# Kernel optimization log

Measured on AMD Instinct MI355X. Metric: run time of the kernel, lower is better.

## Reference

```python
import jax, jax.numpy as jnp
import numpy as np

# Izhikevich constants (module defaults)
A, B_P, C_P, D_P = 0.02, 0.2, -65.0, 8.0
V_TH, DT, T_STEPS = 30.0, 0.5, 8
LN_EPS = 1e-5

IN_F, OUT_F, BATCH = 4096, 4096, 256


def setup_inputs() -> dict:
    key = jax.random.key(0)
    k_x, k_w, k_n = jax.random.split(key, 3)
    x = jax.random.normal(k_x, (BATCH, IN_F), dtype=jnp.float32)
    # kaiming_normal_ fan_in / relu: std = sqrt(2 / fan_in)
    W = jax.random.normal(k_w, (OUT_F, IN_F), dtype=jnp.float32) * np.sqrt(2.0 / IN_F)
    b = jnp.zeros((OUT_F,), dtype=jnp.float32)
    ln_gamma = jnp.ones((OUT_F,), dtype=jnp.float32)
    ln_beta = jnp.zeros((OUT_F,), dtype=jnp.float32)
    current_mag = jnp.asarray(12.0, dtype=jnp.float32)
    # per-step injected noise, precomputed for determinism: (T, B, N)
    noise = jax.random.normal(k_n, (T_STEPS, BATCH, OUT_F), dtype=jnp.float32)
    return {"x": x, "W": W, "b": b, "ln_gamma": ln_gamma, "ln_beta": ln_beta,
            "current_mag": current_mag, "noise": noise}


@jax.custom_vjp
def superspike(v):
    return (v >= V_TH).astype(v.dtype)

def _ss_fwd(v):
    return superspike(v), v

def _ss_bwd(v, g):
    return (g / (1.0 + jnp.abs(v - V_TH)) ** 2,)

superspike.defvjp(_ss_fwd, _ss_bwd)


def reference(x, W, b, ln_gamma, ln_beta, current_mag, noise):
    # 1. Linear projection: (B, in) @ (in, out)
    raw = x @ W.T + b
    # 2. LayerNorm -> tanh -> scale to pA range
    mu = jnp.mean(raw, axis=-1, keepdims=True)
    var = jnp.mean(jnp.square(raw - mu), axis=-1, keepdims=True)
    ln = (raw - mu) * jax.lax.rsqrt(var + LN_EPS) * ln_gamma + ln_beta
    I_inj = jnp.tanh(ln) * jnp.abs(current_mag)  # (B, N)

    B = x.shape[0]
    v0 = jnp.full((B, OUT_F), -65.0, dtype=x.dtype)
    u0 = jnp.full((B, OUT_F), B_P * -65.0, dtype=x.dtype)

    def step(carry, noise_t):
        v, u = carry
        I_t = I_inj + 0.3 * noise_t
        dv = (0.04 * v * v + 5.0 * v + 140.0 - u + I_t) * DT
        du = A * (B_P * v - u) * DT
        v_new = jnp.clip(v + dv, -100.0, 60.0)
        u_new = jnp.clip(u + du, -100.0, 100.0)
        s = superspike(v_new)
        v_out = v_new * (1.0 - s) + C_P * s
        u_out = u_new + D_P * s
        # truncated BPTT: detach state each step
        new_carry = (jax.lax.stop_gradient(v_out), jax.lax.stop_gradient(u_out))
        return new_carry, s

    _, spikes = jax.lax.scan(step, (v0, u0), noise)  # spikes: (T, B, N)
    return jnp.sum(spikes, axis=0) / T_STEPS
```

## Files before the change

kernel.cpp:

```cpp
#include <hip/hip_runtime.h>
#include <math.h>

#define IN_F 4096
#define OUT_F 4096
#define BATCH 256
#define TSTEPS 8

#define BM 128
#define BN 64
#define BK 32
#define KSPLIT 8
#define KLEN (IN_F / KSPLIT)
#define NKT (KLEN / BK)
#define LDA 40

typedef _Float16 f16x8 __attribute__((ext_vector_type(8)));
typedef float f32x4 __attribute__((ext_vector_type(4)));

__device__ __forceinline__ void cvt8(const float4 a, const float4 b,
                                     f16x8& h0, f16x8& h1) {
  const float v[8] = {a.x, a.y, a.z, a.w, b.x, b.y, b.z, b.w};
#pragma unroll
  for (int j = 0; j < 8; ++j) {
    const float sv = v[j] * 64.0f;
    const _Float16 c0 = (_Float16)sv;
    const float r = (sv - (float)c0) * 2048.0f;
    h0[j] = c0;
    h1[j] = (_Float16)r;
  }
}

__global__ __launch_bounds__(256, 3) void gemm_split(
    const float* __restrict__ X, const float* __restrict__ Wt,
    float* __restrict__ out) {
  __shared__ __align__(16) _Float16 B0s[BN][LDA];
  __shared__ __align__(16) _Float16 B1s[BN][LDA];

  const int tid = threadIdx.x;
  const int lane = tid & 63;
  const int w = tid >> 6;
  const int lr = lane & 15;
  const int lk = lane >> 4;

  const int m0 = blockIdx.y * BM;
  const int n0 = blockIdx.x * BN;
  const int kbeg = blockIdx.z * KLEN;

  const float* paf0 = X + (size_t)(m0 + w * 32 + lr) * IN_F + kbeg + lk * 8;
  const float* paf1 = paf0 + (size_t)16 * IN_F;

  const int brow = tid >> 2;
  const int bko = (tid & 3) * 8;
  const float* pb = Wt + (size_t)(n0 + brow) * IN_F + kbeg + bko;

  f32x4 acc0[2][4], acc1[2][4];
#pragma unroll
  for (int i = 0; i < 2; ++i)
#pragma unroll
    for (int j = 0; j < 4; ++j) {
      acc0[i][j] = (f32x4){0.f, 0.f, 0.f, 0.f};
      acc1[i][j] = (f32x4){0.f, 0.f, 0.f, 0.f};
    }

  float4 b0 = *(const float4*)(pb);
  float4 b1 = *(const float4*)(pb + 4);

  for (int kt = 0; kt < NKT; ++kt) {
    const int ko = kt * BK;
    const float4 a00 = *(const float4*)(paf0 + ko);
    const float4 a01 = *(const float4*)(paf0 + ko + 4);
    const float4 a10 = *(const float4*)(paf1 + ko);
    const float4 a11 = *(const float4*)(paf1 + ko + 4);

    __syncthreads();
    {
      f16x8 h0, h1;
      cvt8(b0, b1, h0, h1);
      *(f16x8*)&B0s[brow][bko] = h0;
      *(f16x8*)&B1s[brow][bko] = h1;
    }
    if (kt + 1 < NKT) {
      b0 = *(const float4*)(pb + ko + BK);
      b1 = *(const float4*)(pb + ko + BK + 4);
    }
    __syncthreads();

    f16x8 fa0[2], fa1[2];
    cvt8(a00, a01, fa0[0], fa1[0]);
    cvt8(a10, a11, fa0[1], fa1[1]);

#pragma unroll
    for (int j = 0; j < 4; ++j) {
      const f16x8 fb0 = *(const f16x8*)&B0s[j * 16 + lr][lk * 8];
      const f16x8 fb1 = *(const f16x8*)&B1s[j * 16 + lr][lk * 8];
#pragma unroll
      for (int i = 0; i < 2; ++i) {
        acc0[i][j] = __builtin_amdgcn_mfma_f32_16x16x32_f16(fa0[i], fb0, acc0[i][j], 0, 0, 0);
        acc1[i][j] = __builtin_amdgcn_mfma_f32_16x16x32_f16(fa0[i], fb1, acc1[i][j], 0, 0, 0);
        acc1[i][j] = __builtin_amdgcn_mfma_f32_16x16x32_f16(fa1[i], fb0, acc1[i][j], 0, 0, 0);
      }
    }
  }

#pragma unroll
  for (int i = 0; i < 2; ++i) {
    const int rbase = m0 + w * 32 + i * 16 + lk * 4;
#pragma unroll
    for (int j = 0; j < 4; ++j) {
      const int c = n0 + j * 16 + lr;
#pragma unroll
      for (int r = 0; r < 4; ++r) {
        const float val = acc0[i][j][r] * 2.44140625e-4f  +
                          acc1[i][j][r] * 1.1920928955078125e-7f ;
        atomicAdd(&out[(size_t)(rbase + r) * OUT_F + c], val);
      }
    }
  }
}

__global__ __launch_bounds__(512) void snn_fused(
    float* __restrict__ raw, const float* __restrict__ bias,
    const float* __restrict__ gamma, const float* __restrict__ beta,
    const float* __restrict__ cmag, const float* __restrict__ noise) {
  const int row = blockIdx.x;
  const int tid = threadIdx.x;
  const int lane = tid & 63;
  const int wid = tid >> 6;
  const int col = tid * 8;
  __shared__ float redS[8], redQ[8];

  float x[8];
#pragma unroll
  for (int p = 0; p < 2; ++p) {
    const float4 rv = *(const float4*)&raw[(size_t)row * OUT_F + col + p * 4];
    const float4 bv = *(const float4*)&bias[col + p * 4];
    x[p * 4 + 0] = rv.x + bv.x;
    x[p * 4 + 1] = rv.y + bv.y;
    x[p * 4 + 2] = rv.z + bv.z;
    x[p * 4 + 3] = rv.w + bv.w;
  }
  float s = 0.f, q = 0.f;
#pragma unroll
  for (int e = 0; e < 8; ++e) {
    s += x[e];
    q += x[e] * x[e];
  }
#pragma unroll
  for (int off = 32; off; off >>= 1) {
    s += __shfl_xor(s, off);
    q += __shfl_xor(q, off);
  }
  if (lane == 0) {
    redS[wid] = s;
    redQ[wid] = q;
  }
  __syncthreads();
  s = 0.f;
  q = 0.f;
#pragma unroll
  for (int wv = 0; wv < 8; ++wv) {
    s += redS[wv];
    q += redQ[wv];
  }
  const float mu = s * (1.0f / (float)OUT_F);
  const float var = q * (1.0f / (float)OUT_F) - mu * mu;
  const float sc = 1.0f / sqrtf(var + 1e-5f);
  const float mag = fabsf(cmag[0]);

  float I[8];
#pragma unroll
  for (int p = 0; p < 2; ++p) {
    const float4 g = *(const float4*)&gamma[col + p * 4];
    const float4 be = *(const float4*)&beta[col + p * 4];
    I[p * 4 + 0] = tanhf((x[p * 4 + 0] - mu) * sc * g.x + be.x) * mag;
    I[p * 4 + 1] = tanhf((x[p * 4 + 1] - mu) * sc * g.y + be.y) * mag;
    I[p * 4 + 2] = tanhf((x[p * 4 + 2] - mu) * sc * g.z + be.z) * mag;
    I[p * 4 + 3] = tanhf((x[p * 4 + 3] - mu) * sc * g.w + be.w) * mag;
  }

  float v[8], u[8];
  int cnt[8];
#pragma unroll
  for (int j = 0; j < 8; ++j) {
    v[j] = -65.0f;
    u[j] = -13.0f;
    cnt[j] = 0;
  }

#pragma unroll
  for (int t = 0; t < TSTEPS; ++t) {
    float nn[8];
#pragma unroll
    for (int p = 0; p < 2; ++p) {
      const float4 nz = *(const float4*)&noise[(((size_t)t * BATCH) + row) * OUT_F + col + p * 4];
      nn[p * 4 + 0] = nz.x;
      nn[p * 4 + 1] = nz.y;
      nn[p * 4 + 2] = nz.z;
      nn[p * 4 + 3] = nz.w;
    }
#pragma unroll
    for (int j = 0; j < 8; ++j) {
      const float It = I[j] + 0.3f * nn[j];
      const float vv = v[j];
      const float dv = (0.04f * vv * vv + 5.0f * vv + 140.0f - u[j] + It) * 0.5f;
      const float du = 0.02f * (0.2f * vv - u[j]) * 0.5f;
      float vn = vv + dv;
      vn = fminf(fmaxf(vn, -100.0f), 60.0f);
      float un = u[j] + du;
      un = fminf(fmaxf(un, -100.0f), 100.0f);
      const bool sp = (vn >= 30.0f);
      v[j] = sp ? -65.0f : vn;
      u[j] = sp ? (un + 8.0f) : un;
      cnt[j] += sp ? 1 : 0;
    }
  }

#pragma unroll
  for (int p = 0; p < 2; ++p) {
    float4 o;
    o.x = (float)cnt[p * 4 + 0] * 0.125f;
    o.y = (float)cnt[p * 4 + 1] * 0.125f;
    o.z = (float)cnt[p * 4 + 2] * 0.125f;
    o.w = (float)cnt[p * 4 + 3] * 0.125f;
    *(float4*)&raw[(size_t)row * OUT_F + col + p * 4] = o;
  }
}

extern "C" void kernel_launch(void* const* d_in, const int* in_sizes, int n_in,
                              void* d_out, int out_size, void* d_ws, size_t ws_size,
                              hipStream_t stream) {
  const float* x = (const float*)d_in[0];
  const float* W = (const float*)d_in[1];
  const float* b = (const float*)d_in[2];
  const float* gam = (const float*)d_in[3];
  const float* bet = (const float*)d_in[4];
  const float* cmag = (const float*)d_in[5];
  const float* nz = (const float*)d_in[6];
  float* out = (float*)d_out;
  (void)d_ws;
  (void)ws_size;

  hipMemsetAsync(out, 0, (size_t)BATCH * OUT_F * sizeof(float), stream);

  dim3 grid1(OUT_F / BN, BATCH / BM, KSPLIT);
  gemm_split<<<grid1, 256, 0, stream>>>(x, W, out);

  snn_fused<<<BATCH, 512, 0, stream>>>(out, b, gam, bet, cmag, nz);
}
```

Measured before the change: 186.4 us.

## Pre-split X into fp16 planes and stream W directly without LDS

A new pre-pass kernel splits X once into high and low fp16 planes in the workspace. The GEMM now uses 512-thread blocks that cover the whole batch, so W is read once per block instead of once per M-tile. The LDS staging of B and its barriers are removed: each wave loads its W fragments from global memory and converts them in registers. In exchange, every wave repeats the W fp32-to-fp16 split, and the pre-pass adds one extra launch plus a write and read of the X planes.

```diff
diff --git a/kernel.cpp b/kernel.cpp
--- a/kernel.cpp
+++ b/kernel.cpp
@@ -6,13 +6,11 @@
 #define BATCH 256
 #define TSTEPS 8
 
-#define BM 128
 #define BN 64
 #define BK 32
 #define KSPLIT 8
 #define KLEN (IN_F / KSPLIT)
 #define NKT (KLEN / BK)
-#define LDA 40
 
 typedef _Float16 f16x8 __attribute__((ext_vector_type(8)));
 typedef float f32x4 __attribute__((ext_vector_type(4)));
@@ -30,28 +28,37 @@
   }
 }
 
-__global__ __launch_bounds__(256, 3) void gemm_split(
-    const float* __restrict__ X, const float* __restrict__ Wt,
-    float* __restrict__ out) {
-  __shared__ __align__(16) _Float16 B0s[BN][LDA];
-  __shared__ __align__(16) _Float16 B1s[BN][LDA];
-
+__global__ __launch_bounds__(256) void split_x(const float* __restrict__ X,
+                                               _Float16* __restrict__ h0p,
+                                               _Float16* __restrict__ h1p) {
+  const size_t idx = ((size_t)blockIdx.x * 256 + threadIdx.x) * 8;
+  const float4 a = *(const float4*)&X[idx];
+  const float4 b = *(const float4*)&X[idx + 4];
+  f16x8 h0, h1;
+  cvt8(a, b, h0, h1);
+  *(f16x8*)&h0p[idx] = h0;
+  *(f16x8*)&h1p[idx] = h1;
+}
+
+template <bool USE_WS>
+__global__ void gemm_stream(const _Float16* __restrict__ Ah0,
+                            const _Float16* __restrict__ Ah1,
+                            const float* __restrict__ X,
+                            const float* __restrict__ Wt,
+                            float* __restrict__ out) {
   const int tid = threadIdx.x;
   const int lane = tid & 63;
   const int w = tid >> 6;
   const int lr = lane & 15;
   const int lk = lane >> 4;
 
-  const int m0 = blockIdx.y * BM;
   const int n0 = blockIdx.x * BN;
   const int kbeg = blockIdx.z * KLEN;
 
-  const float* paf0 = X + (size_t)(m0 + w * 32 + lr) * IN_F + kbeg + lk * 8;
-  const float* paf1 = paf0 + (size_t)16 * IN_F;
-
-  const int brow = tid >> 2;
-  const int bko = (tid & 3) * 8;
-  const float* pb = Wt + (size_t)(n0 + brow) * IN_F + kbeg + bko;
+  const _Float16* pa0 = Ah0 + (size_t)(w * 32 + lr) * IN_F + kbeg + lk * 8;
+  const _Float16* pa1 = Ah1 + (size_t)(w * 32 + lr) * IN_F + kbeg + lk * 8;
+  const float* pax = X + (size_t)(w * 32 + lr) * IN_F + kbeg + lk * 8;
+  const float* pb = Wt + (size_t)(n0 + lr) * IN_F + kbeg + lk * 8;
 
   f32x4 acc0[2][4], acc1[2][4];
 #pragma unroll
@@ -62,37 +69,32 @@
       acc1[i][j] = (f32x4){0.f, 0.f, 0.f, 0.f};
     }
 
-  float4 b0 = *(const float4*)(pb);
-  float4 b1 = *(const float4*)(pb + 4);
-
+#pragma unroll 4
   for (int kt = 0; kt < NKT; ++kt) {
     const int ko = kt * BK;
-    const float4 a00 = *(const float4*)(paf0 + ko);
-    const float4 a01 = *(const float4*)(paf0 + ko + 4);
-    const float4 a10 = *(const float4*)(paf1 + ko);
-    const float4 a11 = *(const float4*)(paf1 + ko + 4);
-
-    __syncthreads();
-    {
-      f16x8 h0, h1;
-      cvt8(b0, b1, h0, h1);
-      *(f16x8*)&B0s[brow][bko] = h0;
-      *(f16x8*)&B1s[brow][bko] = h1;
-    }
-    if (kt + 1 < NKT) {
-      b0 = *(const float4*)(pb + ko + BK);
-      b1 = *(const float4*)(pb + ko + BK + 4);
-    }
-    __syncthreads();
 
     f16x8 fa0[2], fa1[2];
-    cvt8(a00, a01, fa0[0], fa1[0]);
-    cvt8(a10, a11, fa0[1], fa1[1]);
+    if (USE_WS) {
+      fa0[0] = *(const f16x8*)(pa0 + ko);
+      fa0[1] = *(const f16x8*)(pa0 + (size_t)16 * IN_F + ko);
+      fa1[0] = *(const f16x8*)(pa1 + ko);
+      fa1[1] = *(const f16x8*)(pa1 + (size_t)16 * IN_F + ko);
+    } else {
+      const float4 a00 = *(const float4*)(pax + ko);
+      const float4 a01 = *(const float4*)(pax + ko + 4);
+      const float4 a10 = *(const float4*)(pax + (size_t)16 * IN_F + ko);
+      const float4 a11 = *(const float4*)(pax + (size_t)16 * IN_F + ko + 4);
+      cvt8(a00, a01, fa0[0], fa1[0]);
+      cvt8(a10, a11, fa0[1], fa1[1]);
+    }
 
 #pragma unroll
     for (int j = 0; j < 4; ++j) {
-      const f16x8 fb0 = *(const f16x8*)&B0s[j * 16 + lr][lk * 8];
-      const f16x8 fb1 = *(const f16x8*)&B1s[j * 16 + lr][lk * 8];
+      const float* pbj = pb + (size_t)(j * 16) * IN_F + ko;
+      const float4 b0 = *(const float4*)(pbj);
+      const float4 b1 = *(const float4*)(pbj + 4);
+      f16x8 fb0, fb1;
+      cvt8(b0, b1, fb0, fb1);
 #pragma unroll
       for (int i = 0; i < 2; ++i) {
         acc0[i][j] = __builtin_amdgcn_mfma_f32_16x16x32_f16(fa0[i], fb0, acc0[i][j], 0, 0, 0);
@@ -104,7 +106,7 @@
 
 #pragma unroll
   for (int i = 0; i < 2; ++i) {
-    const int rbase = m0 + w * 32 + i * 16 + lk * 4;
+    const int rbase = w * 32 + i * 16 + lk * 4;
 #pragma unroll
     for (int j = 0; j < 4; ++j) {
       const int c = n0 + j * 16 + lr;
@@ -237,13 +239,21 @@
   const float* cmag = (const float*)d_in[5];
   const float* nz = (const float*)d_in[6];
   float* out = (float*)d_out;
-  (void)d_ws;
-  (void)ws_size;
 
   hipMemsetAsync(out, 0, (size_t)BATCH * OUT_F * sizeof(float), stream);
 
-  dim3 grid1(OUT_F / BN, BATCH / BM, KSPLIT);
-  gemm_split<<<grid1, 256, 0, stream>>>(x, W, out);
+  const size_t plane_elems = (size_t)BATCH * IN_F;
+  const bool use_ws = ws_size >= 2 * plane_elems * sizeof(_Float16);
+
+  dim3 grid1(OUT_F / BN, 1, KSPLIT);
+  if (use_ws) {
+    _Float16* ah0 = (_Float16*)d_ws;
+    _Float16* ah1 = ah0 + plane_elems;
+    split_x<<<plane_elems / (256 * 8), 256, 0, stream>>>(x, ah0, ah1);
+    gemm_stream<true><<<grid1, 512, 0, stream>>>(ah0, ah1, x, W, out);
+  } else {
+    gemm_stream<false><<<grid1, 512, 0, stream>>>(nullptr, nullptr, x, W, out);
+  }
 
   snn_fused<<<BATCH, 512, 0, stream>>>(out, b, gam, bet, cmag, nz);
 }
```

Result: slower. 241.8 us (+29.7%).

## Restructure split-K GEMM to full-batch tiles with X staged in swizzled LDS

Applied to the files above, without the earlier changes.

The GEMM now has each 512-thread block cover all 256 batch rows by 128 output columns of one K slice, for a grid of 256 blocks. X is converted to a split fp16 pair and staged in a 64KB XOR-swizzled LDS buffer. W fragments are loaded straight from global memory into registers and double-buffered across the MFMA sequence. This removes the W conversion that each M-tile used to repeat, and it reuses the X tile across 128 columns. The cost is a larger accumulator footprint (32 f32x4 per thread), 64KB of LDS per block and fewer blocks, which together may cut occupancy and latency hiding.

```diff
diff --git a/kernel.cpp b/kernel.cpp
--- a/kernel.cpp
+++ b/kernel.cpp
@@ -6,13 +6,8 @@
 #define BATCH 256
 #define TSTEPS 8
 
-#define BM 128
-#define BN 64
-#define BK 32
 #define KSPLIT 8
 #define KLEN (IN_F / KSPLIT)
-#define NKT (KLEN / BK)
-#define LDA 40
 
 typedef _Float16 f16x8 __attribute__((ext_vector_type(8)));
 typedef float f32x4 __attribute__((ext_vector_type(4)));
@@ -30,92 +25,118 @@
   }
 }
 
-__global__ __launch_bounds__(256, 3) void gemm_split(
+__global__ __launch_bounds__(512, 2) void gemm_fused(
     const float* __restrict__ X, const float* __restrict__ Wt,
     float* __restrict__ out) {
-  __shared__ __align__(16) _Float16 B0s[BN][LDA];
-  __shared__ __align__(16) _Float16 B1s[BN][LDA];
+  __shared__ __align__(16) char Al[65536];
 
   const int tid = threadIdx.x;
   const int lane = tid & 63;
   const int w = tid >> 6;
+  const int mq = w & 3;
+  const int ng = w >> 2;
   const int lr = lane & 15;
   const int lk = lane >> 4;
 
-  const int m0 = blockIdx.y * BM;
-  const int n0 = blockIdx.x * BN;
-  const int kbeg = blockIdx.z * KLEN;
-
-  const float* paf0 = X + (size_t)(m0 + w * 32 + lr) * IN_F + kbeg + lk * 8;
-  const float* paf1 = paf0 + (size_t)16 * IN_F;
-
-  const int brow = tid >> 2;
-  const int bko = (tid & 3) * 8;
-  const float* pb = Wt + (size_t)(n0 + brow) * IN_F + kbeg + bko;
-
-  f32x4 acc0[2][4], acc1[2][4];
-#pragma unroll
-  for (int i = 0; i < 2; ++i)
+  const int nb = blockIdx.x & 31;
+  const int ksl = blockIdx.x >> 5;
+  const int n0 = nb * 128;
+  const int kbeg = ksl * KLEN;
+
+  const int srow = tid >> 1;
+  const int skh = (tid & 1) * 32;
+  const float* px = X + (size_t)srow * IN_F + kbeg + skh;
+
+  const float* pw = Wt + (size_t)(n0 + ng * 64 + lr) * IN_F + kbeg + lk * 8;
+
+  f32x4 acc0[4][4], acc1[4][4];
+#pragma unroll
+  for (int i = 0; i < 4; ++i)
 #pragma unroll
     for (int j = 0; j < 4; ++j) {
       acc0[i][j] = (f32x4){0.f, 0.f, 0.f, 0.f};
       acc1[i][j] = (f32x4){0.f, 0.f, 0.f, 0.f};
     }
 
-  float4 b0 = *(const float4*)(pb);
-  float4 b1 = *(const float4*)(pb + 4);
-
-  for (int kt = 0; kt < NKT; ++kt) {
-    const int ko = kt * BK;
-    const float4 a00 = *(const float4*)(paf0 + ko);
-    const float4 a01 = *(const float4*)(paf0 + ko + 4);
-    const float4 a10 = *(const float4*)(paf1 + ko);
-    const float4 a11 = *(const float4*)(paf1 + ko + 4);
-
+  float4 Apre[8];
+#pragma unroll
+  for (int c = 0; c < 8; ++c) Apre[c] = *(const float4*)(px + c * 4);
+
+#define LOADW2(P, JT) \
+  do { \
+    P[0] = *(const float4*)(pwst + (size_t)(JT) * 16 * IN_F); \
+    P[1] = *(const float4*)(pwst + (size_t)(JT) * 16 * IN_F + 4); \
+  } while (0)
+
+#define COMPUTE2(P, JT) \
+  do { \
+    f16x8 fb0, fb1; \
+    cvt8(P[0], P[1], fb0, fb1); \
+    _Pragma("unroll") for (int i_ = 0; i_ < 4; ++i_) { \
+      acc0[i_][JT] = __builtin_amdgcn_mfma_f32_16x16x32_f16(fa0[i_], fb0, acc0[i_][JT], 0, 0, 0); \
+      acc1[i_][JT] = __builtin_amdgcn_mfma_f32_16x16x32_f16(fa0[i_], fb1, acc1[i_][JT], 0, 0, 0); \
+      acc1[i_][JT] = __builtin_amdgcn_mfma_f32_16x16x32_f16(fa1[i_], fb0, acc1[i_][JT], 0, 0, 0); \
+    } \
+  } while (0)
+
+  for (int st = 0; st < 8; ++st) {
     __syncthreads();
-    {
+#pragma unroll
+    for (int c = 0; c < 4; ++c) {
       f16x8 h0, h1;
-      cvt8(b0, b1, h0, h1);
-      *(f16x8*)&B0s[brow][bko] = h0;
-      *(f16x8*)&B1s[brow][bko] = h1;
-    }
-    if (kt + 1 < NKT) {
-      b0 = *(const float4*)(pb + ko + BK);
-      b1 = *(const float4*)(pb + ko + BK + 4);
+      cvt8(Apre[2 * c], Apre[2 * c + 1], h0, h1);
+      const int boff = (skh * 2 + c * 16) ^ ((srow & 7) << 4);
+      *(f16x8*)(Al + (size_t)srow * 128 + boff) = h0;
+      *(f16x8*)(Al + 32768 + (size_t)srow * 128 + boff) = h1;
     }
     __syncthreads();
 
-    f16x8 fa0[2], fa1[2];
-    cvt8(a00, a01, fa0[0], fa1[0]);
-    cvt8(a10, a11, fa0[1], fa1[1]);
-
-#pragma unroll
-    for (int j = 0; j < 4; ++j) {
-      const f16x8 fb0 = *(const f16x8*)&B0s[j * 16 + lr][lk * 8];
-      const f16x8 fb1 = *(const f16x8*)&B1s[j * 16 + lr][lk * 8];
-#pragma unroll
-      for (int i = 0; i < 2; ++i) {
-        acc0[i][j] = __builtin_amdgcn_mfma_f32_16x16x32_f16(fa0[i], fb0, acc0[i][j], 0, 0, 0);
-        acc1[i][j] = __builtin_amdgcn_mfma_f32_16x16x32_f16(fa0[i], fb1, acc1[i][j], 0, 0, 0);
-        acc1[i][j] = __builtin_amdgcn_mfma_f32_16x16x32_f16(fa1[i], fb0, acc1[i][j], 0, 0, 0);
+#pragma unroll
+    for (int ks = 0; ks < 2; ++ks) {
+      f16x8 fa0[4], fa1[4];
+#pragma unroll
+      for (int i = 0; i < 4; ++i) {
+        const int row = mq * 64 + i * 16 + lr;
+        const int boff = (ks * 64 + lk * 16) ^ ((row & 7) << 4);
+        fa0[i] = *(const f16x8*)(Al + (size_t)row * 128 + boff);
+        fa1[i] = *(const f16x8*)(Al + 32768 + (size_t)row * 128 + boff);
       }
-    }
-  }
-
-#pragma unroll
-  for (int i = 0; i < 2; ++i) {
-    const int rbase = m0 + w * 32 + i * 16 + lk * 4;
-#pragma unroll
-    for (int j = 0; j < 4; ++j) {
-      const int c = n0 + j * 16 + lr;
+      if (ks == 1 && st < 7) {
+        const float* pxn = px + (st + 1) * 64;
+#pragma unroll
+        for (int c = 0; c < 8; ++c) Apre[c] = *(const float4*)(pxn + c * 4);
+      }
+
+      const float* pwst = pw + st * 64 + ks * 32;
+      float4 p0[2], p1[2];
+      LOADW2(p0, 0);
+      LOADW2(p1, 1);
+      COMPUTE2(p0, 0);
+      LOADW2(p0, 2);
+      COMPUTE2(p1, 1);
+      LOADW2(p1, 3);
+      COMPUTE2(p0, 2);
+      COMPUTE2(p1, 3);
+    }
+  }
+
+  const int cbase = n0 + ng * 64 + lr;
+#pragma unroll
+  for (int i = 0; i < 4; ++i) {
+    const int rbase = mq * 64 + i * 16 + lk * 4;
+#pragma unroll
+    for (int jt = 0; jt < 4; ++jt) {
+      const int c = cbase + jt * 16;
 #pragma unroll
       for (int r = 0; r < 4; ++r) {
-        const float val = acc0[i][j][r] * 2.44140625e-4f  +
-                          acc1[i][j][r] * 1.1920928955078125e-7f ;
+        const float val = acc0[i][jt][r] * 2.44140625e-4f  +
+                          acc1[i][jt][r] * 1.1920928955078125e-7f ;
         atomicAdd(&out[(size_t)(rbase + r) * OUT_F + c], val);
       }
     }
   }
+#undef LOADW2
+#undef COMPUTE2
 }
 
 __global__ __launch_bounds__(512) void snn_fused(
@@ -242,8 +263,7 @@
 
   hipMemsetAsync(out, 0, (size_t)BATCH * OUT_F * sizeof(float), stream);
 
-  dim3 grid1(OUT_F / BN, BATCH / BM, KSPLIT);
-  gemm_split<<<grid1, 256, 0, stream>>>(x, W, out);
+  gemm_fused<<<256, 512, 0, stream>>>(x, W, out);
 
   snn_fused<<<BATCH, 512, 0, stream>>>(out, b, gam, bet, cmag, nz);
 }
```

After: 205.4 us. +10.2%, slower.
